# Optimization experiments

Measured on AMD Instinct MI355X. Metric: run time of the kernel, lower is better.

## Reference

```python
import jax, jax.numpy as jnp
import numpy as np

N = 4096      # num nodes
F = 64        # input feature dim
H = 8         # head_num
D = 8         # att_embedding_size


def setup_inputs() -> dict:
    key = jax.random.key(0)
    k1, k2, k3, k4, k5, k6 = jax.random.split(key, 6)
    X = jax.random.normal(k1, (N, F), dtype=jnp.float32)
    # sparse-ish binary adjacency with self loops (avg degree ~ 41)
    A = (jax.random.uniform(k2, (N, N)) < 0.01).astype(jnp.float32)
    A = jnp.maximum(A, jnp.eye(N, dtype=jnp.float32))
    # glorot-uniform-ish parameter init
    lim_w = np.sqrt(6.0 / (F + H * D)).astype(np.float32)
    W = jax.random.uniform(k3, (F, H * D), minval=-lim_w, maxval=lim_w, dtype=jnp.float32)
    lim_a = np.sqrt(6.0 / (1 + H * D)).astype(np.float32)
    att_self = jax.random.uniform(k4, (H, D), minval=-lim_a, maxval=lim_a, dtype=jnp.float32)
    att_neigh = jax.random.uniform(k5, (H, D), minval=-lim_a, maxval=lim_a, dtype=jnp.float32)
    bias = jnp.zeros((H, D), dtype=jnp.float32)
    return {"X": X, "A": A, "W": W, "att_self": att_self, "att_neigh": att_neigh, "bias": bias}


def reference(X, A, W, att_self, att_neigh, bias):
    # features: [N, H, D]
    feats = (X @ W).reshape(-1, H, D)
    # additive attention logits per node/head: [N, H]
    a_self = jnp.einsum('nhd,hd->nh', feats, att_self)
    a_neigh = jnp.einsum('nhd,hd->nh', feats, att_neigh)
    # scores[h, i, j] = a_self[i, h] + a_neigh[j, h]  -> [H, N, N]
    scores = a_self.T[:, :, None] + a_neigh.T[:, None, :]
    scores = jax.nn.leaky_relu(scores, negative_slope=0.2)
    # adjacency mask: -1e10 where no edge
    scores = scores + (-1e10 * (1.0 - A))[None, :, :]
    attn = jax.nn.softmax(scores, axis=-1)           # [H, N, N]
    # aggregate: [H, N, N] x [N, H, D] -> [N, H, D]
    out = jnp.einsum('hij,jhd->ihd', attn, feats)
    out = out + bias[None, :, :]                     # use_bias
    out = out.reshape(-1, H * D)                     # reduction='concat'
    return jax.nn.relu(out)                          # activation=relu
```

## Files before the change

### kernel.cpp

```cpp
#include <hip/hip_runtime.h>
#include <hip/hip_bf16.h>

#define NNODES 4096
#define NF 64
#define NH 8
#define ND 8
#define HD 64

__device__ __forceinline__ float ldv(const void* p, int i, bool f32) {
    return f32 ? ((const float*)p)[i]
               : __bfloat162float(((const __hip_bfloat16*)p)[i]);
}

__device__ __forceinline__ bool a_is_f32(const void* A) {
    return *(const unsigned int*)A == 0x3F800000u;
}

__global__ __launch_bounds__(256) void gat_feats(
    const void* __restrict__ X,
    const void* __restrict__ W,
    const void* __restrict__ att_self,
    const void* __restrict__ att_neigh,
    const void* __restrict__ A,
    float* __restrict__ feats,
    float* __restrict__ a_self,
    float* __restrict__ a_neigh)
{
    const bool f32 = a_is_f32(A);
    __shared__ float Wl[NF][HD];
    __shared__ float Xl[4][NF];

    const int t = threadIdx.x;

    #pragma unroll
    for (int k = 0; k < 16; ++k) {
        int idx = t + k * 256;
        Wl[idx >> 6][idx & 63] = ldv(W, idx, f32);
    }

    const int n0 = blockIdx.x * 4;
    const int r = t >> 6;
    const int c = t & 63;
    Xl[r][c] = ldv(X, (n0 + r) * NF + c, f32);
    __syncthreads();

    float acc = 0.f;
    #pragma unroll
    for (int k = 0; k < NF; ++k)
        acc = fmaf(Xl[r][k], Wl[k][c], acc);

    const int n = n0 + r;
    feats[n * HD + c] = acc;

    const int d = c & 7;
    const int h = c >> 3;
    float vs = acc * ldv(att_self, c, f32);
    float vn = acc * ldv(att_neigh, c, f32);
    #pragma unroll
    for (int off = 1; off < 8; off <<= 1) {
        vs += __shfl_xor(vs, off, 64);
        vn += __shfl_xor(vn, off, 64);
    }
    if (d == 0) {
        a_self[n * NH + h]  = vs;
        a_neigh[n * NH + h] = vn;
    }
}

__global__ __launch_bounds__(256) void gat_aggr(
    const void* __restrict__ A,
    const float* __restrict__ feats,
    const float* __restrict__ a_self_g,
    const float* __restrict__ a_neigh,
    const void* __restrict__ bias,
    float* __restrict__ out)
{
    const int i = blockIdx.x;
    const int t = threadIdx.x;
    const bool f32 = a_is_f32(A);
    const int wave = t >> 6, lane = t & 63;

    __shared__ unsigned short elist[NNODES];
    __shared__ int wtot[4];
    __shared__ float red[4][HD];
    __shared__ float dsh[4][NH];

    unsigned int bits = 0;
    if (f32) {
        const uint4* ap = (const uint4*)((const float*)A + (size_t)i * NNODES + t * 16);
        #pragma unroll
        for (int q = 0; q < 4; ++q) {
            uint4 p = ap[q];
            if (p.x) bits |= 1u << (4 * q + 0);
            if (p.y) bits |= 1u << (4 * q + 1);
            if (p.z) bits |= 1u << (4 * q + 2);
            if (p.w) bits |= 1u << (4 * q + 3);
        }
    } else {
        const uint4* ap = (const uint4*)((const unsigned short*)A + (size_t)i * NNODES + t * 16);
        uint4 p0 = ap[0], p1 = ap[1];
        unsigned int w0[4] = {p0.x, p0.y, p0.z, p0.w};
        unsigned int w1[4] = {p1.x, p1.y, p1.z, p1.w};
        #pragma unroll
        for (int q = 0; q < 4; ++q) {
            if (w0[q] & 0x0000ffffu) bits |= 1u << (2 * q);
            if (w0[q] & 0xffff0000u) bits |= 1u << (2 * q + 1);
            if (w1[q] & 0x0000ffffu) bits |= 1u << (8 + 2 * q);
            if (w1[q] & 0xffff0000u) bits |= 1u << (8 + 2 * q + 1);
        }
    }

    int cnt = __popc(bits);
    int incl = cnt;
    #pragma unroll
    for (int off = 1; off < 64; off <<= 1) {
        int nn = __shfl_up(incl, off, 64);
        if (lane >= off) incl += nn;
    }
    if (lane == 63) wtot[wave] = incl;
    __syncthreads();
    int base = 0;
    #pragma unroll
    for (int w = 0; w < 4; ++w) if (w < wave) base += wtot[w];
    const int nE = wtot[0] + wtot[1] + wtot[2] + wtot[3];
    int off0 = base + (incl - cnt);
    unsigned int mb = bits;
    while (mb) {
        int b = __ffs(mb) - 1; mb &= mb - 1;
        elist[off0++] = (unsigned short)(t * 16 + b);
    }
    __syncthreads();

    const int c = lane;
    const int h = c >> 3, d = c & 7;
    const float ash = a_self_g[i * NH + h];
    float acc = 0.f, den = 0.f;

    const int chunk = (nE + 3) >> 2;
    int e = wave * chunk;
    const int eEnd = min(nE, e + chunk);

    for (; e + 8 <= eEnd; e += 8) {
        int j[8];
        #pragma unroll
        for (int k = 0; k < 8; ++k) j[k] = elist[e + k];
        float an[8], fv[8];
        #pragma unroll
        for (int k = 0; k < 8; ++k) an[k] = a_neigh[j[k] * NH + h];
        #pragma unroll
        for (int k = 0; k < 8; ++k) fv[k] = feats[j[k] * HD + c];
        #pragma unroll
        for (int k = 0; k < 8; ++k) {
            float s = ash + an[k];
            s = (s >= 0.f) ? s : 0.2f * s;
            float wt = __expf(s);
            acc = fmaf(wt, fv[k], acc);
            den += wt;
        }
    }
    for (; e + 4 <= eEnd; e += 4) {
        int j[4];
        #pragma unroll
        for (int k = 0; k < 4; ++k) j[k] = elist[e + k];
        float an[4], fv[4];
        #pragma unroll
        for (int k = 0; k < 4; ++k) an[k] = a_neigh[j[k] * NH + h];
        #pragma unroll
        for (int k = 0; k < 4; ++k) fv[k] = feats[j[k] * HD + c];
        #pragma unroll
        for (int k = 0; k < 4; ++k) {
            float s = ash + an[k];
            s = (s >= 0.f) ? s : 0.2f * s;
            float wt = __expf(s);
            acc = fmaf(wt, fv[k], acc);
            den += wt;
        }
    }
    for (; e < eEnd; ++e) {
        int j = elist[e];
        float s = ash + a_neigh[j * NH + h];
        s = (s >= 0.f) ? s : 0.2f * s;
        float wt = __expf(s);
        acc = fmaf(wt, feats[j * HD + c], acc);
        den += wt;
    }

    red[wave][c] = acc;
    if (d == 0) dsh[wave][h] = den;
    __syncthreads();

    if (t < HD) {
        float tot = red[0][t] + red[1][t] + red[2][t] + red[3][t];
        int hh = t >> 3;
        float dd = dsh[0][hh] + dsh[1][hh] + dsh[2][hh] + dsh[3][hh];
        float v = tot / dd + ldv(bias, t, f32);
        out[(size_t)i * HD + t] = fmaxf(v, 0.f);
    }
}

extern "C" void kernel_launch(void* const* d_in, const int* in_sizes, int n_in,
                              void* d_out, int out_size, void* d_ws, size_t ws_size,
                              hipStream_t stream) {
    const void* X         = d_in[0];
    const void* A         = d_in[1];
    const void* W         = d_in[2];
    const void* att_self  = d_in[3];
    const void* att_neigh = d_in[4];
    const void* bias      = d_in[5];
    float* out = (float*)d_out;

    float* feats   = (float*)d_ws;
    float* a_self  = feats  + NNODES * HD;
    float* a_neigh = a_self + NNODES * NH;

    gat_feats<<<NNODES / 4, 256, 0, stream>>>(X, W, att_self, att_neigh, A,
                                              feats, a_self, a_neigh);
    gat_aggr<<<NNODES, 256, 0, stream>>>(A, feats, a_self, a_neigh, bias, out);
}
```

Measured before the change: 28.55 us.

## Split adjacency scan into separate kernel and aggregate one node per wave

Moves the adjacency compaction into its own kernel that writes per-row edge lists and counts to global workspace, then aggregates with one wavefront per node instead of four waves sharing a node through LDS reductions. Edge indices are loaded as packed 16-byte vectors with one-step prefetch, and the W/X loads in the feature kernel are vectorised. This removes the block-level syncs and shared-memory reduction from aggregation and decouples the bandwidth-bound scan from the gather. In exchange it adds a third kernel launch and a round trip of the edge lists through global memory, and the overlap of scan with compute inside one block is lost.

```diff
diff --git a/kernel.cpp b/kernel.cpp
--- a/kernel.cpp
+++ b/kernel.cpp
@@ -6,10 +6,28 @@
 #define NH 8
 #define ND 8
 #define HD 64
+#define ESTRIDE 4096
 
 __device__ __forceinline__ float ldv(const void* p, int i, bool f32) {
     return f32 ? ((const float*)p)[i]
                : __bfloat162float(((const __hip_bfloat16*)p)[i]);
+}
+
+__device__ __forceinline__ void ld8(const void* base, int idx, bool f32, float* o) {
+    if (f32) {
+        const float4* p = (const float4*)((const float*)base + idx);
+        float4 a = p[0], b = p[1];
+        o[0]=a.x; o[1]=a.y; o[2]=a.z; o[3]=a.w;
+        o[4]=b.x; o[5]=b.y; o[6]=b.z; o[7]=b.w;
+    } else {
+        uint4 u = *(const uint4*)((const unsigned short*)base + idx);
+        unsigned int ws[4] = {u.x, u.y, u.z, u.w};
+        #pragma unroll
+        for (int q = 0; q < 4; ++q) {
+            o[2*q]   = __uint_as_float(ws[q] << 16);
+            o[2*q+1] = __uint_as_float(ws[q] & 0xffff0000u);
+        }
+    }
 }
 
 __device__ __forceinline__ bool a_is_f32(const void* A) {
@@ -32,24 +50,32 @@
 
     const int t = threadIdx.x;
 
-    #pragma unroll
-    for (int k = 0; k < 16; ++k) {
-        int idx = t + k * 256;
-        Wl[idx >> 6][idx & 63] = ldv(W, idx, f32);
-    }
-
-    const int n0 = blockIdx.x * 4;
+    {
+        float wv[16];
+        ld8(W, t * 16,     f32, wv);
+        ld8(W, t * 16 + 8, f32, wv + 8);
+        const int row = t >> 2, col0 = (t & 3) * 16;
+        #pragma unroll
+        for (int k = 0; k < 16; ++k) Wl[row][col0 + k] = wv[k];
+    }
+    if (t < 32) {
+        const int row = t >> 3, col = (t & 7) * 8;
+        float xv[8];
+        ld8(X, (blockIdx.x * 4 + row) * NF + col, f32, xv);
+        #pragma unroll
+        for (int k = 0; k < 8; ++k) Xl[row][col + k] = xv[k];
+    }
+    __syncthreads();
+
     const int r = t >> 6;
     const int c = t & 63;
-    Xl[r][c] = ldv(X, (n0 + r) * NF + c, f32);
-    __syncthreads();
 
     float acc = 0.f;
     #pragma unroll
     for (int k = 0; k < NF; ++k)
         acc = fmaf(Xl[r][k], Wl[k][c], acc);
 
-    const int n = n0 + r;
+    const int n = blockIdx.x * 4 + r;
     feats[n * HD + c] = acc;
 
     const int d = c & 7;
@@ -67,23 +93,16 @@
     }
 }
 
-__global__ __launch_bounds__(256) void gat_aggr(
+__global__ __launch_bounds__(256) void gat_scan(
     const void* __restrict__ A,
-    const float* __restrict__ feats,
-    const float* __restrict__ a_self_g,
-    const float* __restrict__ a_neigh,
-    const void* __restrict__ bias,
-    float* __restrict__ out)
+    unsigned short* __restrict__ elist_g,
+    int* __restrict__ ecnt)
 {
     const int i = blockIdx.x;
     const int t = threadIdx.x;
     const bool f32 = a_is_f32(A);
     const int wave = t >> 6, lane = t & 63;
-
-    __shared__ unsigned short elist[NNODES];
     __shared__ int wtot[4];
-    __shared__ float red[4][HD];
-    __shared__ float dsh[4][NH];
 
     unsigned int bits = 0;
     if (f32) {
@@ -122,62 +141,65 @@
     int base = 0;
     #pragma unroll
     for (int w = 0; w < 4; ++w) if (w < wave) base += wtot[w];
-    const int nE = wtot[0] + wtot[1] + wtot[2] + wtot[3];
-    int off0 = base + (incl - cnt);
+
+    int off0 = i * ESTRIDE + base + (incl - cnt);
     unsigned int mb = bits;
     while (mb) {
         int b = __ffs(mb) - 1; mb &= mb - 1;
-        elist[off0++] = (unsigned short)(t * 16 + b);
-    }
-    __syncthreads();
-
-    const int c = lane;
-    const int h = c >> 3, d = c & 7;
+        elist_g[off0++] = (unsigned short)(t * 16 + b);
+    }
+    if (t == 0) ecnt[i] = wtot[0] + wtot[1] + wtot[2] + wtot[3];
+}
+
+__global__ __launch_bounds__(256) void gat_aggr(
+    const unsigned short* __restrict__ elist_g,
+    const int* __restrict__ ecnt,
+    const float* __restrict__ feats,
+    const float* __restrict__ a_self_g,
+    const float* __restrict__ a_neigh,
+    const void* __restrict__ bias,
+    const void* __restrict__ A,
+    float* __restrict__ out)
+{
+    const bool f32 = a_is_f32(A);
+    const int wave = threadIdx.x >> 6, lane = threadIdx.x & 63;
+    const int i = (blockIdx.x << 2) + wave;
+    const int c = lane, h = lane >> 3;
+
     const float ash = a_self_g[i * NH + h];
+    const int nE = ecnt[i];
+    const unsigned short* el = elist_g + (size_t)i * ESTRIDE;
+
     float acc = 0.f, den = 0.f;
-
-    const int chunk = (nE + 3) >> 2;
-    int e = wave * chunk;
-    const int eEnd = min(nE, e + chunk);
-
-    for (; e + 8 <= eEnd; e += 8) {
-        int j[8];
-        #pragma unroll
-        for (int k = 0; k < 8; ++k) j[k] = elist[e + k];
-        float an[8], fv[8];
-        #pragma unroll
-        for (int k = 0; k < 8; ++k) an[k] = a_neigh[j[k] * NH + h];
-        #pragma unroll
-        for (int k = 0; k < 8; ++k) fv[k] = feats[j[k] * HD + c];
-        #pragma unroll
-        for (int k = 0; k < 8; ++k) {
-            float s = ash + an[k];
-            s = (s >= 0.f) ? s : 0.2f * s;
-            float wt = __expf(s);
-            acc = fmaf(wt, fv[k], acc);
-            den += wt;
-        }
-    }
-    for (; e + 4 <= eEnd; e += 4) {
-        int j[4];
-        #pragma unroll
-        for (int k = 0; k < 4; ++k) j[k] = elist[e + k];
-        float an[4], fv[4];
-        #pragma unroll
-        for (int k = 0; k < 4; ++k) an[k] = a_neigh[j[k] * NH + h];
-        #pragma unroll
-        for (int k = 0; k < 4; ++k) fv[k] = feats[j[k] * HD + c];
-        #pragma unroll
-        for (int k = 0; k < 4; ++k) {
-            float s = ash + an[k];
-            s = (s >= 0.f) ? s : 0.2f * s;
-            float wt = __expf(s);
-            acc = fmaf(wt, fv[k], acc);
-            den += wt;
-        }
-    }
-    for (; e < eEnd; ++e) {
-        int j = elist[e];
+    int e = 0;
+
+    if (nE >= 8) {
+        uint4 ev = *(const uint4*)el;
+        for (; e + 8 <= nE; e += 8) {
+            uint4 nx = (e + 16 <= nE) ? *(const uint4*)(el + e + 8) : ev;
+            int j[8];
+            j[0] = ev.x & 0xffff; j[1] = ev.x >> 16;
+            j[2] = ev.y & 0xffff; j[3] = ev.y >> 16;
+            j[4] = ev.z & 0xffff; j[5] = ev.z >> 16;
+            j[6] = ev.w & 0xffff; j[7] = ev.w >> 16;
+            float an[8], fv[8];
+            #pragma unroll
+            for (int k = 0; k < 8; ++k) an[k] = a_neigh[j[k] * NH + h];
+            #pragma unroll
+            for (int k = 0; k < 8; ++k) fv[k] = feats[j[k] * HD + c];
+            #pragma unroll
+            for (int k = 0; k < 8; ++k) {
+                float s = ash + an[k];
+                s = (s >= 0.f) ? s : 0.2f * s;
+                float wt = __expf(s);
+                acc = fmaf(wt, fv[k], acc);
+                den += wt;
+            }
+            ev = nx;
+        }
+    }
+    for (; e < nE; ++e) {
+        int j = el[e];
         float s = ash + a_neigh[j * NH + h];
         s = (s >= 0.f) ? s : 0.2f * s;
         float wt = __expf(s);
@@ -185,17 +207,8 @@
         den += wt;
     }
 
-    red[wave][c] = acc;
-    if (d == 0) dsh[wave][h] = den;
-    __syncthreads();
-
-    if (t < HD) {
-        float tot = red[0][t] + red[1][t] + red[2][t] + red[3][t];
-        int hh = t >> 3;
-        float dd = dsh[0][hh] + dsh[1][hh] + dsh[2][hh] + dsh[3][hh];
-        float v = tot / dd + ldv(bias, t, f32);
-        out[(size_t)i * HD + t] = fmaxf(v, 0.f);
-    }
+    float v = acc / den + ldv(bias, c, f32);
+    out[(size_t)i * HD + c] = fmaxf(v, 0.f);
 }
 
 extern "C" void kernel_launch(void* const* d_in, const int* in_sizes, int n_in,
@@ -212,8 +225,12 @@
     float* feats   = (float*)d_ws;
     float* a_self  = feats  + NNODES * HD;
     float* a_neigh = a_self + NNODES * NH;
+    int*   ecnt    = (int*)(a_neigh + NNODES * NH);
+    unsigned short* elist = (unsigned short*)(ecnt + NNODES);
 
     gat_feats<<<NNODES / 4, 256, 0, stream>>>(X, W, att_self, att_neigh, A,
                                               feats, a_self, a_neigh);
-    gat_aggr<<<NNODES, 256, 0, stream>>>(A, feats, a_self, a_neigh, bias, out);
-}
+    gat_scan<<<NNODES, 256, 0, stream>>>(A, elist, ecnt);
+    gat_aggr<<<NNODES / 4, 256, 0, stream>>>(elist, ecnt, feats, a_self,
+                                             a_neigh, bias, A, out);
+}
```

After: 33.36 us. 1.17x slower.
